# Optimization experiments

Hardware: AMD Instinct MI355X
Metric: run time of the kernel (lower is better)

## Reference

```python
import jax, jax.numpy as jnp
import numpy as np

N = 100000
E = 1600000
BN_EPS = 1e-5
L2_EPS = 1e-12


def _sage_conv(x, src, dst, wl, bl, wr):
    # mean-aggregate source features onto destination nodes
    s = jax.ops.segment_sum(x[src], dst, num_segments=N)          # [N, C]
    cnt = jax.ops.segment_sum(jnp.ones((E,), x.dtype), dst, num_segments=N)
    agg = s / jnp.maximum(cnt, 1.0)[:, None]
    out = agg @ wl.T + bl + x @ wr.T                              # lin_l(agg) + lin_r(x)
    # normalize=True -> row-wise L2 normalization
    nrm = jnp.sqrt(jnp.sum(out * out, axis=-1, keepdims=True))
    return out / jnp.maximum(nrm, L2_EPS)


def _bn(x, g, b):
    # BatchNorm1d, training-mode batch statistics (biased variance)
    m = jnp.mean(x, axis=0)
    v = jnp.mean((x - m) ** 2, axis=0)
    return (x - m) / jnp.sqrt(v + BN_EPS) * g + b


def setup_inputs() -> dict:
    key = jax.random.key(0)
    ks = jax.random.split(key, 24)
    dims = [(4, 6), (6, 8), (8, 16), (16, 32)]
    inp = {
        "x": jax.random.normal(ks[0], (N, 4), jnp.float32),
        "edge_index": jax.random.randint(ks[1], (2, E), 0, N, dtype=jnp.int64),
    }
    ki = 2
    for li, (ci, co) in enumerate(dims, start=1):
        sc = 1.0 / np.sqrt(ci)
        inp[f"w{li}l"] = jax.random.uniform(ks[ki], (co, ci), jnp.float32, -sc, sc); ki += 1
        inp[f"b{li}l"] = jax.random.uniform(ks[ki], (co,), jnp.float32, -sc, sc); ki += 1
        inp[f"w{li}r"] = jax.random.uniform(ks[ki], (co, ci), jnp.float32, -sc, sc); ki += 1
    for li, co in enumerate([6, 8, 16], start=1):
        inp[f"g{li}"] = jnp.ones((co,), jnp.float32)
        inp[f"be{li}"] = jnp.zeros((co,), jnp.float32)
    return inp


def reference(x, edge_index,
              w1l, b1l, w1r, w2l, b2l, w2r, w3l, b3l, w3r, w4l, b4l, w4r,
              g1, be1, g2, be2, g3, be3):
    src, dst = edge_index[0], edge_index[1]
    h = _sage_conv(x, src, dst, w1l, b1l, w1r)
    h = _bn(jax.nn.relu(h), g1, be1)
    h = _sage_conv(h, src, dst, w2l, b2l, w2r)
    h = _bn(jax.nn.relu(h), g2, be2)
    h = _sage_conv(h, src, dst, w3l, b3l, w3r)
    h = _bn(jax.nn.relu(h), g3, be3)
    h = _sage_conv(h, src, dst, w4l, b4l, w4r)
    return jax.nn.relu(h)
```

## Files before the change

### kernel.cpp

```cpp
#include <hip/hip_runtime.h>

#define NNODES 100000
#define NEDGES 1600000
#define BN_EPS 1e-5f
#define L2_EPS 1e-12f

#define BKT_SHIFT 9
#define BKT_SIZE  512
#define NBKT      196
#define CHUNK     8192
#define NBLK_E    196
#define NSLOT     64

template<int NT>
__device__ __forceinline__ int block_excl_scan(int v, int* wsum) {
    __syncthreads();
    constexpr int NW = NT / 64;
    int incl = v;
#pragma unroll
    for (int off = 1; off < 64; off <<= 1) {
        int t = __shfl_up(incl, off);
        if ((threadIdx.x & 63) >= off) incl += t;
    }
    int wid = threadIdx.x >> 6;
    if ((threadIdx.x & 63) == 63) wsum[wid] = incl;
    __syncthreads();
    if (threadIdx.x < NW) {
        int w = wsum[threadIdx.x];
#pragma unroll
        for (int off = 1; off < NW; off <<= 1) {
            int t = __shfl_up(w, off);
            if ((int)threadIdx.x >= off) w += t;
        }
        wsum[threadIdx.x] = w;
    }
    __syncthreads();
    int base = wid ? wsum[wid - 1] : 0;
    return base + incl - v;
}

__global__ void hist_kernel(const int* __restrict__ dst,
                            int* __restrict__ blk_hist_T, float* __restrict__ stats) {
    __shared__ int h[NBKT];
    for (int i = threadIdx.x; i < NBKT; i += blockDim.x) h[i] = 0;
    if (blockIdx.x == 0)
        for (int i = threadIdx.x; i < 3 * NSLOT * 64; i += blockDim.x) stats[i] = 0.0f;
    __syncthreads();
    int base = blockIdx.x * CHUNK;
    int end  = min(base + CHUNK, NEDGES);
    for (int e = base + threadIdx.x * 4; e < end; e += blockDim.x * 4) {
        int4 d = *reinterpret_cast<const int4*>(dst + e);
        atomicAdd(&h[d.x >> BKT_SHIFT], 1);
        atomicAdd(&h[d.y >> BKT_SHIFT], 1);
        atomicAdd(&h[d.z >> BKT_SHIFT], 1);
        atomicAdd(&h[d.w >> BKT_SHIFT], 1);
    }
    __syncthreads();
    for (int i = threadIdx.x; i < NBKT; i += blockDim.x)
        blk_hist_T[i * NBLK_E + blockIdx.x] = h[i];
}

__global__ void scan_blocks(const int* __restrict__ blk_hist_T,
                            int* __restrict__ blk_off, int* __restrict__ bucket_total) {
    __shared__ int wsum[4];
    int b = blockIdx.x;
    int i = threadIdx.x;
    int v = (i < NBLK_E) ? blk_hist_T[b * NBLK_E + i] : 0;
    int excl = block_excl_scan<256>(v, wsum);
    if (i < NBLK_E) blk_off[i * NBKT + b] = excl;
    if (i == 255) bucket_total[b] = excl + v;
}

__global__ void bucket_scatter(const int* __restrict__ src, const int* __restrict__ dst,
                               const int* __restrict__ blk_off, const int* __restrict__ bucket_total,
                               unsigned int* __restrict__ staged) {
    __shared__ int cur[NBKT];
    __shared__ int wsum[8];
    int v = (threadIdx.x < NBKT) ? bucket_total[threadIdx.x] : 0;
    int bbase = block_excl_scan<512>(v, wsum);
    if (threadIdx.x < NBKT)
        cur[threadIdx.x] = bbase + blk_off[blockIdx.x * NBKT + threadIdx.x];
    __syncthreads();
    int base = blockIdx.x * CHUNK;
    int end  = min(base + CHUNK, NEDGES);
    for (int e = base + threadIdx.x * 4; e < end; e += blockDim.x * 4) {
        int4 d = *reinterpret_cast<const int4*>(dst + e);
        int4 s = *reinterpret_cast<const int4*>(src + e);
        int p0 = atomicAdd(&cur[d.x >> BKT_SHIFT], 1);
        staged[p0] = ((unsigned)(d.x & (BKT_SIZE - 1)) << 23) | (unsigned)s.x;
        int p1 = atomicAdd(&cur[d.y >> BKT_SHIFT], 1);
        staged[p1] = ((unsigned)(d.y & (BKT_SIZE - 1)) << 23) | (unsigned)s.y;
        int p2 = atomicAdd(&cur[d.z >> BKT_SHIFT], 1);
        staged[p2] = ((unsigned)(d.z & (BKT_SIZE - 1)) << 23) | (unsigned)s.z;
        int p3 = atomicAdd(&cur[d.w >> BKT_SHIFT], 1);
        staged[p3] = ((unsigned)(d.w & (BKT_SIZE - 1)) << 23) | (unsigned)s.w;
    }
}

__global__ void csr_finalize(const unsigned int* __restrict__ staged,
                             const int* __restrict__ bucket_total,
                             int* __restrict__ row_ptr, int* __restrict__ col) {
    __shared__ int nh[BKT_SIZE];
    __shared__ int cur[BKT_SIZE];
    __shared__ int wsum[8];
    __shared__ int sBeg, sEnd;
    int b = blockIdx.x;

    nh[threadIdx.x] = 0;
    int v = (threadIdx.x < NBKT) ? bucket_total[threadIdx.x] : 0;
    int excl = block_excl_scan<512>(v, wsum);
    if (threadIdx.x == b) { sBeg = excl; sEnd = excl + v; }
    __syncthreads();
    int beg = sBeg, end = sEnd;

    for (int e = beg + threadIdx.x; e < end; e += blockDim.x)
        atomicAdd(&nh[staged[e] >> 23], 1);
    __syncthreads();

    int hv = nh[threadIdx.x];
    int hexcl = block_excl_scan<512>(hv, wsum);

    int node = b * BKT_SIZE + threadIdx.x;
    if (node < NNODES) row_ptr[node] = beg + hexcl;
    if (b == 0 && threadIdx.x == 0) row_ptr[NNODES] = NEDGES;
    cur[threadIdx.x] = hexcl;
    __syncthreads();

    for (int e = beg + threadIdx.x; e < end; e += blockDim.x) {
        unsigned pk = staged[e];
        int l = (int)(pk >> 23);
        int p = atomicAdd(&cur[l], 1);
        col[beg + p] = (int)(pk & 0x7FFFFF);
    }
}

template<int CI>
__device__ __forceinline__ void load_row(const float* __restrict__ p, float* r) {
    constexpr int N4 = CI / 4;
#pragma unroll
    for (int i = 0; i < N4; i++) {
        float4 v = ((const float4*)p)[i];
        r[4*i] = v.x; r[4*i+1] = v.y; r[4*i+2] = v.z; r[4*i+3] = v.w;
    }
    if constexpr ((CI % 4) >= 2) {
        float2 v = ((const float2*)(p + 4 * N4))[0];
        r[4*N4] = v.x; r[4*N4+1] = v.y;
    }
    if constexpr ((CI % 2) == 1) r[CI - 1] = p[CI - 1];
}

template<int CI, int SI, int CO, int SO, int G, bool IN_AFFINE, bool DO_STATS>
__global__ void layer_kernel(const int* __restrict__ row_ptr, const int* __restrict__ col,
                             const float* __restrict__ h,
                             const float* __restrict__ ssum_in, const float* __restrict__ ssq_in,
                             const float* __restrict__ g_in, const float* __restrict__ b_in,
                             const float* __restrict__ wl, const float* __restrict__ bl,
                             const float* __restrict__ wr,
                             float* __restrict__ y,
                             float* __restrict__ stat_sum, float* __restrict__ stat_sq) {
    constexpr int NPB = 256 / G;
    constexpr int OPL = (CO + G - 1) / G;
    constexpr int PCI = CI + 1;

    __shared__ float sWl[CO * PCI];
    __shared__ float sWr[CO * PCI];
    __shared__ float sBl[CO];
    __shared__ float sSc[CI];
    __shared__ float sSh[CI];
    __shared__ float sSumR[CI];
    __shared__ float sSqR[CI];
    __shared__ float red_sum[CO];
    __shared__ float red_sq[CO];

    for (int i = threadIdx.x; i < CO * CI; i += blockDim.x) {
        int o = i / CI, c = i - o * CI;
        sWl[o * PCI + c] = wl[i];
        sWr[o * PCI + c] = wr[i];
    }
    if (threadIdx.x < CO) {
        sBl[threadIdx.x] = bl[threadIdx.x];
        if (DO_STATS) { red_sum[threadIdx.x] = 0.0f; red_sq[threadIdx.x] = 0.0f; }
    }
    if (IN_AFFINE && threadIdx.x < CI) { sSumR[threadIdx.x] = 0.0f; sSqR[threadIdx.x] = 0.0f; }
    __syncthreads();
    if (IN_AFFINE) {
        int c = threadIdx.x & 31, sl = threadIdx.x >> 5;
        if (c < CI) {
            float ps = 0.0f, pq = 0.0f;
#pragma unroll
            for (int s = sl; s < NSLOT; s += 8) {
                ps += ssum_in[s * 64 + c];
                pq += ssq_in[s * 64 + c];
            }
            atomicAdd(&sSumR[c], ps);
            atomicAdd(&sSqR[c], pq);
        }
        __syncthreads();
        if (threadIdx.x < CI) {
            float m  = sSumR[threadIdx.x] * (1.0f / NNODES);
            float vv = sSqR[threadIdx.x] * (1.0f / NNODES) - m * m;
            float s  = g_in[threadIdx.x] / sqrtf(vv + BN_EPS);
            sSc[threadIdx.x] = s;
            sSh[threadIdx.x] = b_in[threadIdx.x] - m * s;
        }
    }
    __syncthreads();

    int node = blockIdx.x * NPB + (threadIdx.x / G);
    int g    = threadIdx.x & (G - 1);
    bool valid = node < NNODES;

    float acc[CI];
#pragma unroll
    for (int c = 0; c < CI; c++) acc[c] = 0.0f;

    int beg = 0, end = 0;
    if (valid) {
        beg = row_ptr[node];
        end = row_ptr[node + 1];
        int j = beg + g;
        if constexpr (G <= 8) {
            for (; j + 3 * G < end; j += 4 * G) {
                int i0 = col[j], i1 = col[j + G], i2 = col[j + 2 * G], i3 = col[j + 3 * G];
                float r0[CI], r1[CI], r2[CI], r3[CI];
                load_row<CI>(h + (long)i0 * SI, r0);
                load_row<CI>(h + (long)i1 * SI, r1);
                load_row<CI>(h + (long)i2 * SI, r2);
                load_row<CI>(h + (long)i3 * SI, r3);
#pragma unroll
                for (int c = 0; c < CI; c++) acc[c] += (r0[c] + r1[c]) + (r2[c] + r3[c]);
            }
        }
        for (; j + G < end; j += 2 * G) {
            int i0 = col[j], i1 = col[j + G];
            float r0[CI], r1[CI];
            load_row<CI>(h + (long)i0 * SI, r0);
            load_row<CI>(h + (long)i1 * SI, r1);
#pragma unroll
            for (int c = 0; c < CI; c++) acc[c] += r0[c] + r1[c];
        }
        if (j < end) {
            float r0[CI];
            load_row<CI>(h + (long)col[j] * SI, r0);
#pragma unroll
            for (int c = 0; c < CI; c++) acc[c] += r0[c];
        }
    }

#pragma unroll
    for (int m = 1; m < G; m <<= 1)
#pragma unroll
        for (int c = 0; c < CI; c++) acc[c] += __shfl_xor(acc[c], m);

    float out[OPL];
    float nrm2 = 0.0f;
    if (valid) {
        float ic = 1.0f / fmaxf((float)(end - beg), 1.0f);
        float xin[CI];
        load_row<CI>(h + (long)node * SI, xin);
        float agg[CI];
#pragma unroll
        for (int c = 0; c < CI; c++) {
            float a  = acc[c] * ic;
            float xv = xin[c];
            if (IN_AFFINE) {
                a  = a  * sSc[c] + sSh[c];
                xv = xv * sSc[c] + sSh[c];
            }
            agg[c] = a;
            xin[c] = xv;
        }
#pragma unroll
        for (int k = 0; k < OPL; k++) {
            int o = g * OPL + k;
            float v = 0.0f;
            if (o < CO) {
                v = sBl[o];
#pragma unroll
                for (int c = 0; c < CI; c++)
                    v += sWl[o * PCI + c] * agg[c] + sWr[o * PCI + c] * xin[c];
            }
            out[k] = v;
            nrm2 += v * v;
        }
    }
#pragma unroll
    for (int m = 1; m < G; m <<= 1) nrm2 += __shfl_xor(nrm2, m);

    if (valid) {
        float inv_nrm = 1.0f / fmaxf(sqrtf(nrm2), L2_EPS);
#pragma unroll
        for (int k = 0; k < OPL; k++) {
            int o = g * OPL + k;
            if (o < CO) {
                float v = fmaxf(out[k] * inv_nrm, 0.0f);
                y[(long)node * SO + o] = v;
                if (DO_STATS) {
                    atomicAdd(&red_sum[o], v);
                    atomicAdd(&red_sq[o], v * v);
                }
            }
        }
    }

    if (DO_STATS) {
        __syncthreads();
        if (threadIdx.x < CO) {
            int slot = blockIdx.x & (NSLOT - 1);
            atomicAdd(&stat_sum[slot * 64 + threadIdx.x], red_sum[threadIdx.x]);
            atomicAdd(&stat_sq [slot * 64 + threadIdx.x], red_sq[threadIdx.x]);
        }
    }
}

extern "C" void kernel_launch(void* const* d_in, const int* in_sizes, int n_in,
                              void* d_out, int out_size, void* d_ws, size_t ws_size,
                              hipStream_t stream) {
    const float* x   = (const float*)d_in[0];
    const int*   ei  = (const int*)d_in[1];
    const int*   src = ei;
    const int*   dst = ei + NEDGES;

    const float* w1l = (const float*)d_in[2];
    const float* b1l = (const float*)d_in[3];
    const float* w1r = (const float*)d_in[4];
    const float* w2l = (const float*)d_in[5];
    const float* b2l = (const float*)d_in[6];
    const float* w2r = (const float*)d_in[7];
    const float* w3l = (const float*)d_in[8];
    const float* b3l = (const float*)d_in[9];
    const float* w3r = (const float*)d_in[10];
    const float* w4l = (const float*)d_in[11];
    const float* b4l = (const float*)d_in[12];
    const float* w4r = (const float*)d_in[13];
    const float* g1  = (const float*)d_in[14];
    const float* be1 = (const float*)d_in[15];
    const float* g2  = (const float*)d_in[16];
    const float* be2 = (const float*)d_in[17];
    const float* g3  = (const float*)d_in[18];
    const float* be3 = (const float*)d_in[19];

    char* w = (char*)d_ws;
    int* blk_hist     = (int*)w;  w += NBLK_E * NBKT * 4;
    int* blk_off      = (int*)w;  w += NBLK_E * NBKT * 4;
    int* bucket_total = (int*)w;  w += 256 * 4;
    int* row_ptr      = (int*)w;  w += (NNODES + 8) * 4;
    int* col          = (int*)w;  w += NEDGES * 4;
    float* hA         = (float*)w; w += NNODES * 16 * 4;
    float* hB         = (float*)w; w += NNODES * 16 * 4;
    float* stats      = (float*)w; w += 3 * NSLOT * 64 * 4;
    unsigned int* staged = (unsigned int*)hB;

    float* ssum1 = stats + 0 * NSLOT * 64, *ssq1 = ssum1 + 32;
    float* ssum2 = stats + 1 * NSLOT * 64, *ssq2 = ssum2 + 32;
    float* ssum3 = stats + 2 * NSLOT * 64, *ssq3 = ssum3 + 32;

    hist_kernel   <<<NBLK_E, 512, 0, stream>>>(dst, blk_hist, stats);
    scan_blocks   <<<NBKT, 256, 0, stream>>>(blk_hist, blk_off, bucket_total);
    bucket_scatter<<<NBLK_E, 512, 0, stream>>>(src, dst, blk_off, bucket_total, staged);
    csr_finalize  <<<NBKT, 512, 0, stream>>>(staged, bucket_total, row_ptr, col);

    layer_kernel<4, 4, 6, 8, 8, false, true><<<(NNODES * 8 + 255) / 256, 256, 0, stream>>>(
        row_ptr, col, x, nullptr, nullptr, nullptr, nullptr,
        w1l, b1l, w1r, hA, ssum1, ssq1);

    layer_kernel<6, 8, 8, 8, 8, true, true><<<(NNODES * 8 + 255) / 256, 256, 0, stream>>>(
        row_ptr, col, hA, ssum1, ssq1, g1, be1,
        w2l, b2l, w2r, hB, ssum2, ssq2);

    layer_kernel<8, 8, 16, 16, 8, true, true><<<(NNODES * 8 + 255) / 256, 256, 0, stream>>>(
        row_ptr, col, hB, ssum2, ssq2, g2, be2,
        w3l, b3l, w3r, hA, ssum3, ssq3);

    layer_kernel<16, 16, 32, 32, 16, true, false><<<(NNODES * 16 + 255) / 256, 256, 0, stream>>>(
        row_ptr, col, hA, ssum3, ssq3, g3, be3,
        w4l, b4l, w4r, (float*)d_out, nullptr, nullptr);
}
```

Before: 260.0 us.

## Use edge-parallel aggregation with shared-memory atomics per 64-node block

Replaces the per-node grouped gather, where G lanes walk each node's neighbour list, with an edge-parallel scheme. Each block of 64 nodes spreads its contiguous CSR edge range across all 256 threads and accumulates into shared memory with atomics. The local destination index is packed into the upper bits of col during CSR finalize, so no per-edge search is needed. The aim is to remove load imbalance from varying degrees and idle lanes, at the cost of shared-memory atomic contention and a 4-threads-per-node epilogue.

```diff
diff --git a/kernel.cpp b/kernel.cpp
--- a/kernel.cpp
+++ b/kernel.cpp
@@ -11,6 +11,8 @@
 #define CHUNK     8192
 #define NBLK_E    196
 #define NSLOT     64
+#define NPB       64
+#define SRCMASK   0x03FFFFFFu
 
 template<int NT>
 __device__ __forceinline__ int block_excl_scan(int v, int* wsum) {
@@ -99,7 +101,7 @@
 
 __global__ void csr_finalize(const unsigned int* __restrict__ staged,
                              const int* __restrict__ bucket_total,
-                             int* __restrict__ row_ptr, int* __restrict__ col) {
+                             int* __restrict__ row_ptr, unsigned int* __restrict__ col) {
     __shared__ int nh[BKT_SIZE];
     __shared__ int cur[BKT_SIZE];
     __shared__ int wsum[8];
@@ -130,7 +132,7 @@
         unsigned pk = staged[e];
         int l = (int)(pk >> 23);
         int p = atomicAdd(&cur[l], 1);
-        col[beg + p] = (int)(pk & 0x7FFFFF);
+        col[beg + p] = ((unsigned)(l & (NPB - 1)) << 26) | (pk & 0x7FFFFF);
     }
 }
 
@@ -149,8 +151,8 @@
     if constexpr ((CI % 2) == 1) r[CI - 1] = p[CI - 1];
 }
 
-template<int CI, int SI, int CO, int SO, int G, bool IN_AFFINE, bool DO_STATS>
-__global__ void layer_kernel(const int* __restrict__ row_ptr, const int* __restrict__ col,
+template<int CI, int SI, int CO, int SO, bool IN_AFFINE, bool DO_STATS>
+__global__ void layer_kernel(const int* __restrict__ row_ptr, const unsigned int* __restrict__ col,
                              const float* __restrict__ h,
                              const float* __restrict__ ssum_in, const float* __restrict__ ssq_in,
                              const float* __restrict__ g_in, const float* __restrict__ b_in,
@@ -158,33 +160,38 @@
                              const float* __restrict__ wr,
                              float* __restrict__ y,
                              float* __restrict__ stat_sum, float* __restrict__ stat_sq) {
-    constexpr int NPB = 256 / G;
-    constexpr int OPL = (CO + G - 1) / G;
-    constexpr int PCI = CI + 1;
-
-    __shared__ float sWl[CO * PCI];
-    __shared__ float sWr[CO * PCI];
+    constexpr int CIp = CI + 1;
+    constexpr int OPT = (CO + 3) / 4;
+
+    __shared__ float acc[NPB * CIp];
+    __shared__ float sWl[CO * CIp];
+    __shared__ float sWr[CO * CIp];
     __shared__ float sBl[CO];
     __shared__ float sSc[CI];
     __shared__ float sSh[CI];
+    __shared__ int   sRP[NPB + 1];
     __shared__ float sSumR[CI];
     __shared__ float sSqR[CI];
     __shared__ float red_sum[CO];
     __shared__ float red_sq[CO];
 
-    for (int i = threadIdx.x; i < CO * CI; i += blockDim.x) {
+    int tid = threadIdx.x;
+    for (int i = tid; i < CO * CI; i += 256) {
         int o = i / CI, c = i - o * CI;
-        sWl[o * PCI + c] = wl[i];
-        sWr[o * PCI + c] = wr[i];
-    }
-    if (threadIdx.x < CO) {
-        sBl[threadIdx.x] = bl[threadIdx.x];
-        if (DO_STATS) { red_sum[threadIdx.x] = 0.0f; red_sq[threadIdx.x] = 0.0f; }
-    }
-    if (IN_AFFINE && threadIdx.x < CI) { sSumR[threadIdx.x] = 0.0f; sSqR[threadIdx.x] = 0.0f; }
+        sWl[o * CIp + c] = wl[i];
+        sWr[o * CIp + c] = wr[i];
+    }
+    if (tid < CO) {
+        sBl[tid] = bl[tid];
+        if (DO_STATS) { red_sum[tid] = 0.0f; red_sq[tid] = 0.0f; }
+    }
+    for (int i = tid; i < NPB * CIp; i += 256) acc[i] = 0.0f;
+    int first = blockIdx.x * NPB;
+    if (tid <= NPB) sRP[tid] = row_ptr[min(first + tid, NNODES)];
+    if (IN_AFFINE && tid < CI) { sSumR[tid] = 0.0f; sSqR[tid] = 0.0f; }
     __syncthreads();
     if (IN_AFFINE) {
-        int c = threadIdx.x & 31, sl = threadIdx.x >> 5;
+        int c = tid & 31, sl = tid >> 5;
         if (c < CI) {
             float ps = 0.0f, pq = 0.0f;
 #pragma unroll
@@ -196,108 +203,99 @@
             atomicAdd(&sSqR[c], pq);
         }
         __syncthreads();
-        if (threadIdx.x < CI) {
-            float m  = sSumR[threadIdx.x] * (1.0f / NNODES);
-            float vv = sSqR[threadIdx.x] * (1.0f / NNODES) - m * m;
-            float s  = g_in[threadIdx.x] / sqrtf(vv + BN_EPS);
-            sSc[threadIdx.x] = s;
-            sSh[threadIdx.x] = b_in[threadIdx.x] - m * s;
-        }
-    }
-    __syncthreads();
-
-    int node = blockIdx.x * NPB + (threadIdx.x / G);
-    int g    = threadIdx.x & (G - 1);
+        if (tid < CI) {
+            float m  = sSumR[tid] * (1.0f / NNODES);
+            float vv = sSqR[tid] * (1.0f / NNODES) - m * m;
+            float s  = g_in[tid] / sqrtf(vv + BN_EPS);
+            sSc[tid] = s;
+            sSh[tid] = b_in[tid] - m * s;
+        }
+        __syncthreads();
+    }
+
+    int ebeg = sRP[0], eend = sRP[NPB];
+    int e = ebeg + tid;
+    for (; e + 3 * 256 < eend; e += 4 * 256) {
+        unsigned v0 = col[e], v1 = col[e + 256], v2 = col[e + 512], v3 = col[e + 768];
+        float r0[CI], r1[CI], r2[CI], r3[CI];
+        load_row<CI>(h + (long)(v0 & SRCMASK) * SI, r0);
+        load_row<CI>(h + (long)(v1 & SRCMASK) * SI, r1);
+        load_row<CI>(h + (long)(v2 & SRCMASK) * SI, r2);
+        load_row<CI>(h + (long)(v3 & SRCMASK) * SI, r3);
+        int d0 = (int)(v0 >> 26) * CIp, d1 = (int)(v1 >> 26) * CIp;
+        int d2 = (int)(v2 >> 26) * CIp, d3 = (int)(v3 >> 26) * CIp;
+#pragma unroll
+        for (int c = 0; c < CI; c++) atomicAdd(&acc[d0 + c], r0[c]);
+#pragma unroll
+        for (int c = 0; c < CI; c++) atomicAdd(&acc[d1 + c], r1[c]);
+#pragma unroll
+        for (int c = 0; c < CI; c++) atomicAdd(&acc[d2 + c], r2[c]);
+#pragma unroll
+        for (int c = 0; c < CI; c++) atomicAdd(&acc[d3 + c], r3[c]);
+    }
+    for (; e < eend; e += 256) {
+        unsigned v0 = col[e];
+        float r0[CI];
+        load_row<CI>(h + (long)(v0 & SRCMASK) * SI, r0);
+        int d0 = (int)(v0 >> 26) * CIp;
+#pragma unroll
+        for (int c = 0; c < CI; c++) atomicAdd(&acc[d0 + c], r0[c]);
+    }
+    __syncthreads();
+
+    int nl = tid >> 2, t = tid & 3;
+    int node = first + nl;
     bool valid = node < NNODES;
 
-    float acc[CI];
-#pragma unroll
-    for (int c = 0; c < CI; c++) acc[c] = 0.0f;
-
-    int beg = 0, end = 0;
-    if (valid) {
-        beg = row_ptr[node];
-        end = row_ptr[node + 1];
-        int j = beg + g;
-        if constexpr (G <= 8) {
-            for (; j + 3 * G < end; j += 4 * G) {
-                int i0 = col[j], i1 = col[j + G], i2 = col[j + 2 * G], i3 = col[j + 3 * G];
-                float r0[CI], r1[CI], r2[CI], r3[CI];
-                load_row<CI>(h + (long)i0 * SI, r0);
-                load_row<CI>(h + (long)i1 * SI, r1);
-                load_row<CI>(h + (long)i2 * SI, r2);
-                load_row<CI>(h + (long)i3 * SI, r3);
-#pragma unroll
-                for (int c = 0; c < CI; c++) acc[c] += (r0[c] + r1[c]) + (r2[c] + r3[c]);
-            }
-        }
-        for (; j + G < end; j += 2 * G) {
-            int i0 = col[j], i1 = col[j + G];
-            float r0[CI], r1[CI];
-            load_row<CI>(h + (long)i0 * SI, r0);
-            load_row<CI>(h + (long)i1 * SI, r1);
-#pragma unroll
-            for (int c = 0; c < CI; c++) acc[c] += r0[c] + r1[c];
-        }
-        if (j < end) {
-            float r0[CI];
-            load_row<CI>(h + (long)col[j] * SI, r0);
-#pragma unroll
-            for (int c = 0; c < CI; c++) acc[c] += r0[c];
-        }
-    }
-
-#pragma unroll
-    for (int m = 1; m < G; m <<= 1)
-#pragma unroll
-        for (int c = 0; c < CI; c++) acc[c] += __shfl_xor(acc[c], m);
-
-    float out[OPL];
+    float outv[OPT];
     float nrm2 = 0.0f;
     if (valid) {
-        float ic = 1.0f / fmaxf((float)(end - beg), 1.0f);
-        float xin[CI];
+        int deg = sRP[nl + 1] - sRP[nl];
+        float ic = 1.0f / fmaxf((float)deg, 1.0f);
+        float a[CI], xin[CI];
         load_row<CI>(h + (long)node * SI, xin);
-        float agg[CI];
 #pragma unroll
         for (int c = 0; c < CI; c++) {
-            float a  = acc[c] * ic;
+            float av = acc[nl * CIp + c] * ic;
             float xv = xin[c];
             if (IN_AFFINE) {
-                a  = a  * sSc[c] + sSh[c];
+                av = av * sSc[c] + sSh[c];
                 xv = xv * sSc[c] + sSh[c];
             }
-            agg[c] = a;
+            a[c] = av;
             xin[c] = xv;
         }
 #pragma unroll
-        for (int k = 0; k < OPL; k++) {
-            int o = g * OPL + k;
+        for (int k = 0; k < OPT; k++) {
+            int o = t * OPT + k;
             float v = 0.0f;
             if (o < CO) {
                 v = sBl[o];
 #pragma unroll
                 for (int c = 0; c < CI; c++)
-                    v += sWl[o * PCI + c] * agg[c] + sWr[o * PCI + c] * xin[c];
+                    v += sWl[o * CIp + c] * a[c] + sWr[o * CIp + c] * xin[c];
             }
-            out[k] = v;
+            outv[k] = v;
             nrm2 += v * v;
         }
     }
-#pragma unroll
-    for (int m = 1; m < G; m <<= 1) nrm2 += __shfl_xor(nrm2, m);
+    nrm2 += __shfl_xor(nrm2, 1);
+    nrm2 += __shfl_xor(nrm2, 2);
 
     if (valid) {
         float inv_nrm = 1.0f / fmaxf(sqrtf(nrm2), L2_EPS);
-#pragma unroll
-        for (int k = 0; k < OPL; k++) {
-            int o = g * OPL + k;
+        float st[OPT];
+#pragma unroll
+        for (int k = 0; k < OPT; k++) st[k] = fmaxf(outv[k] * inv_nrm, 0.0f);
+        float* yp = y + (long)node * SO + t * OPT;
+#pragma unroll
+        for (int k = 0; k < OPT; k++) {
+            int o = t * OPT + k;
             if (o < CO) {
-                float v = fmaxf(out[k] * inv_nrm, 0.0f);
-                y[(long)node * SO + o] = v;
+                yp[k] = st[k];
                 if (DO_STATS) {
-                    atomicAdd(&red_sum[o], v);
-                    atomicAdd(&red_sq[o], v * v);
+                    atomicAdd(&red_sum[o], st[k]);
+                    atomicAdd(&red_sq[o], st[k] * st[k]);
                 }
             }
         }
@@ -305,10 +303,10 @@
 
     if (DO_STATS) {
         __syncthreads();
-        if (threadIdx.x < CO) {
+        if (tid < CO) {
             int slot = blockIdx.x & (NSLOT - 1);
-            atomicAdd(&stat_sum[slot * 64 + threadIdx.x], red_sum[threadIdx.x]);
-            atomicAdd(&stat_sq [slot * 64 + threadIdx.x], red_sq[threadIdx.x]);
+            atomicAdd(&stat_sum[slot * 64 + tid], red_sum[tid]);
+            atomicAdd(&stat_sq [slot * 64 + tid], red_sq[tid]);
         }
     }
 }
@@ -345,7 +343,7 @@
     int* blk_off      = (int*)w;  w += NBLK_E * NBKT * 4;
     int* bucket_total = (int*)w;  w += 256 * 4;
     int* row_ptr      = (int*)w;  w += (NNODES + 8) * 4;
-    int* col          = (int*)w;  w += NEDGES * 4;
+    unsigned int* col = (unsigned int*)w; w += NEDGES * 4;
     float* hA         = (float*)w; w += NNODES * 16 * 4;
     float* hB         = (float*)w; w += NNODES * 16 * 4;
     float* stats      = (float*)w; w += 3 * NSLOT * 64 * 4;
@@ -360,19 +358,21 @@
     bucket_scatter<<<NBLK_E, 512, 0, stream>>>(src, dst, blk_off, bucket_total, staged);
     csr_finalize  <<<NBKT, 512, 0, stream>>>(staged, bucket_total, row_ptr, col);
 
-    layer_kernel<4, 4, 6, 8, 8, false, true><<<(NNODES * 8 + 255) / 256, 256, 0, stream>>>(
+    const int NLBLK = (NNODES + NPB - 1) / NPB;
+
+    layer_kernel<4, 4, 6, 8, false, true><<<NLBLK, 256, 0, stream>>>(
         row_ptr, col, x, nullptr, nullptr, nullptr, nullptr,
         w1l, b1l, w1r, hA, ssum1, ssq1);
 
-    layer_kernel<6, 8, 8, 8, 8, true, true><<<(NNODES * 8 + 255) / 256, 256, 0, stream>>>(
+    layer_kernel<6, 8, 8, 8, true, true><<<NLBLK, 256, 0, stream>>>(
         row_ptr, col, hA, ssum1, ssq1, g1, be1,
         w2l, b2l, w2r, hB, ssum2, ssq2);
 
-    layer_kernel<8, 8, 16, 16, 8, true, true><<<(NNODES * 8 + 255) / 256, 256, 0, stream>>>(
+    layer_kernel<8, 8, 16, 16, true, true><<<NLBLK, 256, 0, stream>>>(
         row_ptr, col, hB, ssum2, ssq2, g2, be2,
         w3l, b3l, w3r, hA, ssum3, ssq3);
 
-    layer_kernel<16, 16, 32, 32, 16, true, false><<<(NNODES * 16 + 255) / 256, 256, 0, stream>>>(
+    layer_kernel<16, 16, 32, 32, true, false><<<NLBLK, 256, 0, stream>>>(
         row_ptr, col, hA, ssum3, ssq3, g3, be3,
         w4l, b4l, w4r, (float*)d_out, nullptr, nullptr);
 }
```

Result: slower. 647.0 us (+148.9%).

## Store intermediate node features in fp16 and halve layer-4 group size

Applied to the files above, without the earlier changes.

Intermediate hidden activations between layers are now written and read as fp16 in packed 16-byte rows, roughly halving the bytes moved by the random gather over edges. Accumulation, the linear maps, normalization and statistics stay in fp32. Layer 4 now uses 8 threads per node instead of 16, with the 4-way unrolled gather enabled based on channel count. The cost is reduced activation precision, which may affect accuracy tolerance.

```diff
diff --git a/kernel.cpp b/kernel.cpp
--- a/kernel.cpp
+++ b/kernel.cpp
@@ -1,4 +1,5 @@
 #include <hip/hip_runtime.h>
+#include <hip/hip_fp16.h>
 
 #define NNODES 100000
 #define NEDGES 1600000
@@ -134,29 +135,47 @@
     }
 }
 
-template<int CI>
-__device__ __forceinline__ void load_row(const float* __restrict__ p, float* r) {
-    constexpr int N4 = CI / 4;
-#pragma unroll
-    for (int i = 0; i < N4; i++) {
-        float4 v = ((const float4*)p)[i];
-        r[4*i] = v.x; r[4*i+1] = v.y; r[4*i+2] = v.z; r[4*i+3] = v.w;
-    }
-    if constexpr ((CI % 4) >= 2) {
-        float2 v = ((const float2*)(p + 4 * N4))[0];
-        r[4*N4] = v.x; r[4*N4+1] = v.y;
-    }
-    if constexpr ((CI % 2) == 1) r[CI - 1] = p[CI - 1];
-}
-
-template<int CI, int SI, int CO, int SO, int G, bool IN_AFFINE, bool DO_STATS>
+__device__ __forceinline__ void unpack8(uint4 v, float* f) {
+    float2 a = __half22float2(*(const __half2*)&v.x);
+    float2 b = __half22float2(*(const __half2*)&v.y);
+    float2 c = __half22float2(*(const __half2*)&v.z);
+    float2 d = __half22float2(*(const __half2*)&v.w);
+    f[0] = a.x; f[1] = a.y; f[2] = b.x; f[3] = b.y;
+    f[4] = c.x; f[5] = c.y; f[6] = d.x; f[7] = d.y;
+}
+
+template<int CI, int SI, bool H>
+__device__ __forceinline__ void load_row2(const void* base, long node, float* r) {
+    if constexpr (H) {
+        const __half* p = (const __half*)base + node * SI;
+        float t[SI > 8 ? 16 : 8];
+        uint4 v0 = *(const uint4*)p;
+        unpack8(v0, t);
+        if constexpr (SI > 8) {
+            uint4 v1 = *(const uint4*)(p + 8);
+            unpack8(v1, t + 8);
+        }
+#pragma unroll
+        for (int c = 0; c < CI; c++) r[c] = t[c];
+    } else {
+        const float* p = (const float*)base + node * SI;
+#pragma unroll
+        for (int c = 0; c < CI; c += 4) {
+            float4 v = *(const float4*)(p + c);
+            r[c] = v.x; r[c+1] = v.y; r[c+2] = v.z; r[c+3] = v.w;
+        }
+    }
+}
+
+template<int CI, int SI, int CO, int SO, int G,
+         bool IN_HALF, bool OUT_HALF, bool IN_AFFINE, bool DO_STATS>
 __global__ void layer_kernel(const int* __restrict__ row_ptr, const int* __restrict__ col,
-                             const float* __restrict__ h,
+                             const void* __restrict__ h,
                              const float* __restrict__ ssum_in, const float* __restrict__ ssq_in,
                              const float* __restrict__ g_in, const float* __restrict__ b_in,
                              const float* __restrict__ wl, const float* __restrict__ bl,
                              const float* __restrict__ wr,
-                             float* __restrict__ y,
+                             void* __restrict__ y,
                              float* __restrict__ stat_sum, float* __restrict__ stat_sq) {
     constexpr int NPB = 256 / G;
     constexpr int OPL = (CO + G - 1) / G;
@@ -219,14 +238,14 @@
         beg = row_ptr[node];
         end = row_ptr[node + 1];
         int j = beg + g;
-        if constexpr (G <= 8) {
+        if constexpr (CI <= 8) {
             for (; j + 3 * G < end; j += 4 * G) {
                 int i0 = col[j], i1 = col[j + G], i2 = col[j + 2 * G], i3 = col[j + 3 * G];
                 float r0[CI], r1[CI], r2[CI], r3[CI];
-                load_row<CI>(h + (long)i0 * SI, r0);
-                load_row<CI>(h + (long)i1 * SI, r1);
-                load_row<CI>(h + (long)i2 * SI, r2);
-                load_row<CI>(h + (long)i3 * SI, r3);
+                load_row2<CI, SI, IN_HALF>(h, i0, r0);
+                load_row2<CI, SI, IN_HALF>(h, i1, r1);
+                load_row2<CI, SI, IN_HALF>(h, i2, r2);
+                load_row2<CI, SI, IN_HALF>(h, i3, r3);
 #pragma unroll
                 for (int c = 0; c < CI; c++) acc[c] += (r0[c] + r1[c]) + (r2[c] + r3[c]);
             }
@@ -234,14 +253,14 @@
         for (; j + G < end; j += 2 * G) {
             int i0 = col[j], i1 = col[j + G];
             float r0[CI], r1[CI];
-            load_row<CI>(h + (long)i0 * SI, r0);
-            load_row<CI>(h + (long)i1 * SI, r1);
+            load_row2<CI, SI, IN_HALF>(h, i0, r0);
+            load_row2<CI, SI, IN_HALF>(h, i1, r1);
 #pragma unroll
             for (int c = 0; c < CI; c++) acc[c] += r0[c] + r1[c];
         }
         if (j < end) {
             float r0[CI];
-            load_row<CI>(h + (long)col[j] * SI, r0);
+            load_row2<CI, SI, IN_HALF>(h, col[j], r0);
 #pragma unroll
             for (int c = 0; c < CI; c++) acc[c] += r0[c];
         }
@@ -257,7 +276,7 @@
     if (valid) {
         float ic = 1.0f / fmaxf((float)(end - beg), 1.0f);
         float xin[CI];
-        load_row<CI>(h + (long)node * SI, xin);
+        load_row2<CI, SI, IN_HALF>(h, node, xin);
         float agg[CI];
 #pragma unroll
         for (int c = 0; c < CI; c++) {
@@ -292,13 +311,15 @@
 #pragma unroll
         for (int k = 0; k < OPL; k++) {
             int o = g * OPL + k;
-            if (o < CO) {
-                float v = fmaxf(out[k] * inv_nrm, 0.0f);
-                y[(long)node * SO + o] = v;
-                if (DO_STATS) {
-                    atomicAdd(&red_sum[o], v);
-                    atomicAdd(&red_sq[o], v * v);
-                }
+            float v = (o < CO) ? fmaxf(out[k] * inv_nrm, 0.0f) : 0.0f;
+            if constexpr (OUT_HALF) {
+                if (o < SO) ((__half*)y)[(long)node * SO + o] = __float2half_rn(v);
+            } else {
+                if (o < CO) ((float*)y)[(long)node * SO + o] = v;
+            }
+            if (DO_STATS && o < CO) {
+                atomicAdd(&red_sum[o], v);
+                atomicAdd(&red_sq[o], v * v);
             }
         }
     }
@@ -346,8 +367,8 @@
     int* bucket_total = (int*)w;  w += 256 * 4;
     int* row_ptr      = (int*)w;  w += (NNODES + 8) * 4;
     int* col          = (int*)w;  w += NEDGES * 4;
-    float* hA         = (float*)w; w += NNODES * 16 * 4;
-    float* hB         = (float*)w; w += NNODES * 16 * 4;
+    __half* hA        = (__half*)w; w += NNODES * 16 * 4;
+    __half* hB        = (__half*)w; w += NNODES * 16 * 4;
     float* stats      = (float*)w; w += 3 * NSLOT * 64 * 4;
     unsigned int* staged = (unsigned int*)hB;
 
@@ -360,19 +381,21 @@
     bucket_scatter<<<NBLK_E, 512, 0, stream>>>(src, dst, blk_off, bucket_total, staged);
     csr_finalize  <<<NBKT, 512, 0, stream>>>(staged, bucket_total, row_ptr, col);
 
-    layer_kernel<4, 4, 6, 8, 8, false, true><<<(NNODES * 8 + 255) / 256, 256, 0, stream>>>(
+    const int NLB = (NNODES * 8 + 255) / 256;
+
+    layer_kernel<4, 4, 6, 8, 8, false, true, false, true><<<NLB, 256, 0, stream>>>(
         row_ptr, col, x, nullptr, nullptr, nullptr, nullptr,
         w1l, b1l, w1r, hA, ssum1, ssq1);
 
-    layer_kernel<6, 8, 8, 8, 8, true, true><<<(NNODES * 8 + 255) / 256, 256, 0, stream>>>(
+    layer_kernel<6, 8, 8, 8, 8, true, true, true, true><<<NLB, 256, 0, stream>>>(
         row_ptr, col, hA, ssum1, ssq1, g1, be1,
         w2l, b2l, w2r, hB, ssum2, ssq2);
 
-    layer_kernel<8, 8, 16, 16, 8, true, true><<<(NNODES * 8 + 255) / 256, 256, 0, stream>>>(
+    layer_kernel<8, 8, 16, 16, 8, true, true, true, true><<<NLB, 256, 0, stream>>>(
         row_ptr, col, hB, ssum2, ssq2, g2, be2,
         w3l, b3l, w3r, hA, ssum3, ssq3);
 
-    layer_kernel<16, 16, 32, 32, 16, true, false><<<(NNODES * 16 + 255) / 256, 256, 0, stream>>>(
+    layer_kernel<16, 16, 32, 32, 8, true, false, true, false><<<NLB, 256, 0, stream>>>(
         row_ptr, col, hA, ssum3, ssq3, g3, be3,
-        w4l, b4l, w4r, (float*)d_out, nullptr, nullptr);
-}
+        w4l, b4l, w4r, d_out, nullptr, nullptr);
+}
```

Result: faster. 240.1 us (median of 2 runs) (-7.6%).
